# Kernel tuning notes

Measured on AMD Instinct MI355X. Metric: run time of the kernel, lower is better.

## Reference

```python
import jax, jax.numpy as jnp
import numpy as np

N_HEADS = 8
ROPE_BASE = 10000.0


def _rope(x, pos):
    # x: (BN, T, H, D); pos: (T,)
    D = x.shape[-1]
    inv_freq = 1.0 / (ROPE_BASE ** (jnp.arange(0, D, 2, dtype=jnp.float32) / D))  # (D/2,)
    ang = pos[:, None].astype(jnp.float32) * inv_freq[None, :]                    # (T, D/2)
    cos = jnp.concatenate([jnp.cos(ang), jnp.cos(ang)], axis=-1)[None, :, None, :]  # (1,T,1,D)
    sin = jnp.concatenate([jnp.sin(ang), jnp.sin(ang)], axis=-1)[None, :, None, :]
    x1, x2 = x[..., : D // 2], x[..., D // 2 :]
    rot = jnp.concatenate([-x2, x1], axis=-1)
    return x * cos + rot * sin


def setup_inputs() -> dict:
    key = jax.random.key(0)
    ks = jax.random.split(key, 5)
    B, T, N, E = 2, 1024, 4, 256
    s = 1.0 / np.sqrt(E)
    return {
        "input_tensor": jax.random.normal(ks[0], (B, T, N, E), dtype=jnp.float32),
        "w_attn": jax.random.normal(ks[1], (E, 3 * E), dtype=jnp.float32) * s,
        "b_attn": jnp.zeros((3 * E,), dtype=jnp.float32),
        "w_proj": jax.random.normal(ks[2], (E, E), dtype=jnp.float32) * s,
        "b_proj": jnp.zeros((E,), dtype=jnp.float32),
    }


def reference(input_tensor, w_attn, b_attn, w_proj, b_proj):
    B, T, N, E = input_tensor.shape
    H = N_HEADS
    D = E // H
    # (B,T,N,E) -> (B*N, T, E)
    x = jnp.transpose(input_tensor, (0, 2, 1, 3)).reshape(B * N, T, E)
    qkv = x @ w_attn + b_attn  # (BN, T, 3E)
    q, k, v = jnp.split(qkv, 3, axis=-1)
    q = q.reshape(B * N, T, H, D)
    k = k.reshape(B * N, T, H, D)
    v = v.reshape(B * N, T, H, D)
    pos = jnp.arange(T)
    q = _rope(q, pos)
    k = _rope(k, pos)
    # causal SDPA
    scale = 1.0 / jnp.sqrt(jnp.asarray(D, dtype=q.dtype))
    scores = jnp.einsum("bthd,bshd->bhts", q, k) * scale  # (BN,H,T,T)
    causal = jnp.tril(jnp.ones((T, T), dtype=bool))
    scores = jnp.where(causal[None, None], scores, jnp.finfo(scores.dtype).min)
    probs = jax.nn.softmax(scores, axis=-1)
    out = jnp.einsum("bhts,bshd->bthd", probs, v).reshape(B * N, T, E)
    out = out @ w_proj + b_proj
    # (BN,T,E) -> (B,T,N,E)
    return jnp.transpose(out.reshape(B, N, T, E), (0, 2, 1, 3))
```

## Files before the change

kernel.cpp:

```cpp
#include <hip/hip_runtime.h>
#include <hip/hip_bf16.h>

#define T_ 1024
#define NB 4
#define E_ 256
#define H_ 8
#define D_ 32
#define E3 768

typedef __attribute__((ext_vector_type(4))) short v4s;
typedef __attribute__((ext_vector_type(8))) short v8s;
typedef __attribute__((ext_vector_type(4))) float v4f;

#define EXP2F(x) __builtin_amdgcn_exp2f(x)

__device__ __forceinline__ unsigned short f2bf(float x) {
    union { float f; unsigned int u; } v; v.f = x;
    unsigned int r = v.u + 0x7fffu + ((v.u >> 16) & 1u);
    return (unsigned short)(r >> 16);
}
__device__ __forceinline__ unsigned int cvtpk(float lo, float hi) {
    unsigned int r;
    asm("v_cvt_pk_bf16_f32 %0, %1, %2" : "=v"(r) : "v"(lo), "v"(hi));
    return r;
}

__global__ __launch_bounds__(256) void prep_kernel(
    const float* __restrict__ w_attn, const float* __restrict__ w_proj,
    unsigned short* __restrict__ WT, unsigned short* __restrict__ WPT,
    float* __restrict__ ctab, float* __restrict__ stab)
{
    const int blk = blockIdx.x;
    if (blk < 256) {
        __shared__ float tile[32][33];
        const int bx = blk & 31, by = blk >> 5;
        const float* src; unsigned short* dst; int N, n0;
        if (bx < 24) { src = w_attn; dst = WT;  N = 768; n0 = bx * 32; }
        else         { src = w_proj; dst = WPT; N = 256; n0 = (bx - 24) * 32; }
        const int k0 = by * 32;
        const int xx = threadIdx.x & 31, y4 = (threadIdx.x >> 5) * 4;
        #pragma unroll
        for (int i = 0; i < 4; ++i)
            tile[y4 + i][xx] = src[(size_t)(k0 + y4 + i) * N + n0 + xx];
        __syncthreads();
        #pragma unroll
        for (int i = 0; i < 4; ++i)
            dst[(size_t)(n0 + y4 + i) * 256 + k0 + xx] = f2bf(tile[xx][y4 + i]);
    } else {
        const int idx = (blk - 256) * 256 + threadIdx.x;
        const int t = idx >> 4, jj = idx & 15;
        const float invf = __expf(-(float)jj * 0.5756462732485115f);
        float s, c;
        sincosf((float)t * invf, &s, &c);
        ctab[idx] = c;
        stab[idx] = s;
    }
}

__global__ __launch_bounds__(256) void qkv_mfma_kernel(
    const float* __restrict__ x,
    const float* __restrict__ b_attn,
    const unsigned short* __restrict__ WT,
    const float* __restrict__ ctab, const float* __restrict__ stab,
    unsigned short* __restrict__ Qb, unsigned short* __restrict__ Kb,
    unsigned short* __restrict__ VW)
{
    const int tid  = threadIdx.x;
    const int wsb  = tid >> 6;
    const int lane = tid & 63;
    const int g = lane >> 4, c = lane & 15;
    const int m0 = blockIdx.x * 64 + wsb * 16;
    const int n0 = blockIdx.y * 64;
    const int bn = m0 >> 10;
    const int b  = bn >> 2, nidx = bn & 3;
    const int t_base = m0 & 1023;

    const float* xrow = x + ((size_t)(b * T_ + t_base + c) * NB + nidx) * E_;

    v4f acc[4];
    #pragma unroll
    for (int tt = 0; tt < 4; ++tt) acc[tt] = (v4f){0.f, 0.f, 0.f, 0.f};

    #pragma unroll
    for (int k0 = 0; k0 < 256; k0 += 32) {
        float4 f0 = *(const float4*)(xrow + k0 + 8 * g);
        float4 f1 = *(const float4*)(xrow + k0 + 8 * g + 4);
        union { v8s v; uint4 u; } af;
        af.u.x = cvtpk(f0.x, f0.y);
        af.u.y = cvtpk(f0.z, f0.w);
        af.u.z = cvtpk(f1.x, f1.y);
        af.u.w = cvtpk(f1.z, f1.w);
        #pragma unroll
        for (int tt = 0; tt < 4; ++tt) {
            v8s bfrag = *(const v8s*)(WT + (size_t)(n0 + tt * 16 + c) * 256 + k0 + 8 * g);
            acc[tt] = __builtin_amdgcn_mfma_f32_16x16x32_bf16(af.v, bfrag, acc[tt], 0, 0, 0);
        }
    }

    float bias[4];
    #pragma unroll
    for (int tt = 0; tt < 4; ++tt) bias[tt] = b_attn[n0 + tt * 16 + c];

    const int type = n0 >> 8;
    const int nl0  = n0 & 255;

    if (type <= 1) {
        unsigned short* Dst = (type == 0) ? Qb : Kb;
        float sn[4], cs[4];
        #pragma unroll
        for (int r = 0; r < 4; ++r) {
            const int ti = (t_base + 4 * g + r) * 16 + c;
            cs[r] = ctab[ti];
            sn[r] = stab[ti];
        }
        #pragma unroll
        for (int tt = 0; tt < 4; ++tt) {
            const int n_l = nl0 + tt * 16;
            const int h = n_l >> 5, d = (n_l & 31) + c;
            const int bh = bn * 8 + h;
            const float sgn = (tt & 1) ? 1.f : -1.f;
            const int  ptt = tt ^ 1;
            #pragma unroll
            for (int r = 0; r < 4; ++r) {
                float v0 = acc[tt][r] + bias[tt];
                float v1 = acc[ptt][r] + bias[ptt];
                float o  = v0 * cs[r] + sgn * v1 * sn[r];
                int   t  = t_base + 4 * g + r;
                Dst[((size_t)bh * T_ + t) * D_ + d] = f2bf(o);
            }
        }
    } else {
        const int wv_ = t_base >> 5;
        const int tw  = (t_base & 31) + 4 * g;
        const int pos0 = ((tw >> 4) & 1) * 4 + ((tw >> 2) & 3) * 8;
        #pragma unroll
        for (int tt = 0; tt < 4; ++tt) {
            const int n_l = nl0 + tt * 16;
            const int h = n_l >> 5, d = (n_l & 31) + c;
            const int bh = bn * 8 + h;
            ushort4 pk;
            pk.x = f2bf(acc[tt][0] + bias[tt]);
            pk.y = f2bf(acc[tt][1] + bias[tt]);
            pk.z = f2bf(acc[tt][2] + bias[tt]);
            pk.w = f2bf(acc[tt][3] + bias[tt]);
            *(ushort4*)(VW + (((size_t)bh * 32 + wv_) * 32 + d) * 32 + pos0) = pk;
        }
    }
}

#define KMUL   0.2550343f
#define SHIFTL 11.5415603f

__global__ __launch_bounds__(256) void attn_kernel(
    const unsigned short* __restrict__ Qb,
    const unsigned short* __restrict__ Kb,
    const unsigned short* __restrict__ VW,
    unsigned short* __restrict__ Ob)
{
    const int tid  = threadIdx.x;
    const int wv   = tid >> 6;
    const int lane = tid & 63;
    const int g = lane >> 4, c = lane & 15;
    const int bx = blockIdx.x;
    const int bh = bx & 63;
    const int k  = bx >> 6;

    const int qts[2] = { k + 8 * wv, k + 56 - 8 * wv };
    const int lim1 = qts[1] >> 1;

    v8s qf[2];
    #pragma unroll
    for (int j = 0; j < 2; ++j)
        qf[j] = *(const v8s*)(Qb + ((size_t)bh * T_ + qts[j] * 16 + c) * D_ + 8 * g);

    v4f o0[2], o1[2];
    float ll[2];
    #pragma unroll
    for (int j = 0; j < 2; ++j) {
        o0[j] = (v4f){0.f, 0.f, 0.f, 0.f};
        o1[j] = (v4f){0.f, 0.f, 0.f, 0.f};
        ll[j] = 0.f;
    }

    const unsigned short* Ksrc = Kb + (size_t)bh * T_ * D_;
    const unsigned short* Vsrc = VW + (size_t)bh * 32 * 1024;

    const int koff = c * 32 + 8 * g;
    const int voff = c * 32 + 8 * g;

    v8s kA_n  = *(const v8s*)(Ksrc + koff);
    v8s kB_n  = *(const v8s*)(Ksrc + 512 + koff);
    v8s vf0_n = *(const v8s*)(Vsrc + voff);
    v8s vf1_n = *(const v8s*)(Vsrc + 512 + voff);

    for (int w = 0; w <= lim1; ++w) {
        v8s kfA = kA_n, kfB = kB_n;
        v8s vf0 = vf0_n, vf1 = vf1_n;
        if (w < lim1) {
            const unsigned short* kp = Ksrc + (size_t)(w + 1) * 1024;
            const unsigned short* vp = Vsrc + (size_t)(w + 1) * 1024;
            kA_n  = *(const v8s*)(kp + koff);
            kB_n  = *(const v8s*)(kp + 512 + koff);
            vf0_n = *(const v8s*)(vp + voff);
            vf1_n = *(const v8s*)(vp + 512 + voff);
        }

        const int s0 = w * 32;
        #pragma unroll
        for (int j = 0; j < 2; ++j) {
            const int qt  = qts[j];
            const int lim = qt >> 1;
            if (lim < w) continue;
            const int q = qt * 16 + c;

            v4f zero = {0.f, 0.f, 0.f, 0.f};
            v4f sA = __builtin_amdgcn_mfma_f32_16x16x32_bf16(kfA, qf[j], zero, 0, 0, 0);
            v4f sB = __builtin_amdgcn_mfma_f32_16x16x32_bf16(kfB, qf[j], zero, 0, 0, 0);

            const bool diag = (lim == w);
            float p[8];
            #pragma unroll
            for (int r = 0; r < 4; ++r) {
                float pa = EXP2F(fmaf(sA[r], KMUL, -SHIFTL));
                float pb = EXP2F(fmaf(sB[r], KMUL, -SHIFTL));
                if (diag) {
                    if (s0 + 4 * g + r > q)      pa = 0.f;
                    if (s0 + 16 + 4 * g + r > q) pb = 0.f;
                }
                p[r] = pa; p[4 + r] = pb;
                ll[j] += pa + pb;
            }
            union { v8s v; uint4 u; } pu;
            pu.u.x = cvtpk(p[0], p[1]);
            pu.u.y = cvtpk(p[2], p[3]);
            pu.u.z = cvtpk(p[4], p[5]);
            pu.u.w = cvtpk(p[6], p[7]);
            o0[j] = __builtin_amdgcn_mfma_f32_16x16x32_bf16(pu.v, vf0, o0[j], 0, 0, 0);
            o1[j] = __builtin_amdgcn_mfma_f32_16x16x32_bf16(pu.v, vf1, o1[j], 0, 0, 0);
        }
    }

    const int bn = bh >> 3, h = bh & 7;
    #pragma unroll
    for (int j = 0; j < 2; ++j) {
        float l_s = ll[j];
        l_s += __shfl_xor(l_s, 16, 64);
        l_s += __shfl_xor(l_s, 32, 64);
        float linv = 1.0f / l_s;
        float lr[4];
        #pragma unroll
        for (int r = 0; r < 4; ++r) lr[r] = __shfl(linv, 4 * g + r, 64);
        const int q0 = qts[j] * 16;
        #pragma unroll
        for (int r = 0; r < 4; ++r) {
            unsigned short* Orow = Ob + ((size_t)bn * T_ + q0 + 4 * g + r) * E_ + h * D_;
            Orow[c]      = f2bf(o0[j][r] * lr[r]);
            Orow[16 + c] = f2bf(o1[j][r] * lr[r]);
        }
    }
}

__global__ __launch_bounds__(256) void proj_mfma_kernel(
    const unsigned short* __restrict__ Ob,
    const unsigned short* __restrict__ WPT,
    const float* __restrict__ b_proj,
    float* __restrict__ out)
{
    const int tid  = threadIdx.x;
    const int wsb  = tid >> 6;
    const int lane = tid & 63;
    const int g = lane >> 4, c = lane & 15;
    const int m0 = blockIdx.x * 64 + wsb * 16;
    const int n0 = blockIdx.y * 64;
    const int bn = m0 >> 10;
    const int b  = bn >> 2, nidx = bn & 3;
    const int t_base = m0 & 1023;

    const unsigned short* arow = Ob + ((size_t)bn * T_ + t_base + c) * E_;

    v4f acc[4];
    #pragma unroll
    for (int tt = 0; tt < 4; ++tt) acc[tt] = (v4f){0.f, 0.f, 0.f, 0.f};

    #pragma unroll
    for (int s = 0; s < 8; ++s) {
        v8s afrag = *(const v8s*)(arow + s * 32 + 8 * g);
        #pragma unroll
        for (int tt = 0; tt < 4; ++tt) {
            v8s bfrag = *(const v8s*)(WPT + (size_t)(n0 + tt * 16 + c) * 256 + s * 32 + 8 * g);
            acc[tt] = __builtin_amdgcn_mfma_f32_16x16x32_bf16(afrag, bfrag, acc[tt], 0, 0, 0);
        }
    }

    #pragma unroll
    for (int tt = 0; tt < 4; ++tt) {
        const int n = n0 + tt * 16 + c;
        const float bp = b_proj[n];
        #pragma unroll
        for (int r = 0; r < 4; ++r) {
            const int t = t_base + 4 * g + r;
            out[((size_t)(b * T_ + t) * NB + nidx) * E_ + n] = acc[tt][r] + bp;
        }
    }
}

extern "C" void kernel_launch(void* const* d_in, const int* in_sizes, int n_in,
                              void* d_out, int out_size, void* d_ws, size_t ws_size,
                              hipStream_t stream)
{
    const float* x      = (const float*)d_in[0];
    const float* w_attn = (const float*)d_in[1];
    const float* b_attn = (const float*)d_in[2];
    const float* w_proj = (const float*)d_in[3];
    const float* b_proj = (const float*)d_in[4];
    float* out = (float*)d_out;

    unsigned short* Qb  = (unsigned short*)d_ws;
    unsigned short* Kb  = Qb + 2097152;
    unsigned short* VW  = Kb + 2097152;
    unsigned short* Ob  = VW + 2097152;
    unsigned short* WT  = Ob + 2097152;
    unsigned short* WPT = WT + 196608;
    float* ctab = (float*)(WPT + 65536);
    float* stab = ctab + 16384;

    prep_kernel<<<320, 256, 0, stream>>>(w_attn, w_proj, WT, WPT, ctab, stab);
    qkv_mfma_kernel<<<dim3(128, 12), 256, 0, stream>>>(x, b_attn, WT, ctab, stab, Qb, Kb, VW);
    attn_kernel<<<512, 256, 0, stream>>>(Qb, Kb, VW, Ob);
    proj_mfma_kernel<<<dim3(128, 4), 256, 0, stream>>>(Ob, WPT, b_proj, out);
}
```

Baseline: 131.2 us.

## Fuse QKV, attention and projection into one persistent kernel with grid barriers

Merges the QKV GEMM, causal attention and output projection into a single 512-block kernel separated by atomic-counter grid barriers, with the counters reset in the prep kernel. Each block in the QKV phase now computes three 64-column groups, reusing the converted x fragment across them. The goal is to remove two kernel launch gaps and tail effects. In exchange it relies on all 512 blocks being co-resident (launch_bounds 256,2) to avoid deadlock, and it adds spin-wait barrier overhead and more accumulator registers.

```diff
diff --git a/kernel.cpp b/kernel.cpp
--- a/kernel.cpp
+++ b/kernel.cpp
@@ -7,6 +7,7 @@
 #define H_ 8
 #define D_ 32
 #define E3 768
+#define NBLK 512u
 
 typedef __attribute__((ext_vector_type(4))) short v4s;
 typedef __attribute__((ext_vector_type(8))) short v8s;
@@ -25,12 +26,28 @@
     return r;
 }
 
+__device__ __forceinline__ void grid_barrier(unsigned int* cnt) {
+    __syncthreads();
+    __threadfence();
+    if (threadIdx.x == 0) {
+        atomicAdd(cnt, 1u);
+        while (atomicAdd(cnt, 0u) < NBLK) __builtin_amdgcn_s_sleep(2);
+    }
+    __syncthreads();
+    __threadfence();
+}
+
+#define KMUL   0.2550343f
+#define SHIFTL 11.5415603f
+
 __global__ __launch_bounds__(256) void prep_kernel(
     const float* __restrict__ w_attn, const float* __restrict__ w_proj,
     unsigned short* __restrict__ WT, unsigned short* __restrict__ WPT,
-    float* __restrict__ ctab, float* __restrict__ stab)
+    float* __restrict__ ctab, float* __restrict__ stab,
+    unsigned int* __restrict__ cnt)
 {
     const int blk = blockIdx.x;
+    if (blk == 0 && threadIdx.x < 8) cnt[threadIdx.x] = 0u;
     if (blk < 256) {
         __shared__ float tile[32][33];
         const int bx = blk & 31, by = blk >> 5;
@@ -57,55 +74,55 @@
     }
 }
 
-__global__ __launch_bounds__(256) void qkv_mfma_kernel(
+__global__ __launch_bounds__(256, 2) void fused_kernel(
     const float* __restrict__ x,
-    const float* __restrict__ b_attn,
-    const unsigned short* __restrict__ WT,
+    const float* __restrict__ b_attn, const float* __restrict__ b_proj,
+    const unsigned short* __restrict__ WT, const unsigned short* __restrict__ WPT,
     const float* __restrict__ ctab, const float* __restrict__ stab,
     unsigned short* __restrict__ Qb, unsigned short* __restrict__ Kb,
-    unsigned short* __restrict__ VW)
+    unsigned short* __restrict__ VW, unsigned short* __restrict__ Ob,
+    unsigned int* __restrict__ cnt,
+    float* __restrict__ out)
 {
-    const int tid  = threadIdx.x;
+    const int bx  = blockIdx.x;
+    const int tid = threadIdx.x;
     const int wsb  = tid >> 6;
     const int lane = tid & 63;
     const int g = lane >> 4, c = lane & 15;
-    const int m0 = blockIdx.x * 64 + wsb * 16;
-    const int n0 = blockIdx.y * 64;
-    const int bn = m0 >> 10;
-    const int b  = bn >> 2, nidx = bn & 3;
-    const int t_base = m0 & 1023;
-
-    const float* xrow = x + ((size_t)(b * T_ + t_base + c) * NB + nidx) * E_;
-
-    v4f acc[4];
-    #pragma unroll
-    for (int tt = 0; tt < 4; ++tt) acc[tt] = (v4f){0.f, 0.f, 0.f, 0.f};
-
-    #pragma unroll
-    for (int k0 = 0; k0 < 256; k0 += 32) {
-        float4 f0 = *(const float4*)(xrow + k0 + 8 * g);
-        float4 f1 = *(const float4*)(xrow + k0 + 8 * g + 4);
-        union { v8s v; uint4 u; } af;
-        af.u.x = cvtpk(f0.x, f0.y);
-        af.u.y = cvtpk(f0.z, f0.w);
-        af.u.z = cvtpk(f1.x, f1.y);
-        af.u.w = cvtpk(f1.z, f1.w);
-        #pragma unroll
-        for (int tt = 0; tt < 4; ++tt) {
-            v8s bfrag = *(const v8s*)(WT + (size_t)(n0 + tt * 16 + c) * 256 + k0 + 8 * g);
-            acc[tt] = __builtin_amdgcn_mfma_f32_16x16x32_bf16(af.v, bfrag, acc[tt], 0, 0, 0);
-        }
-    }
-
-    float bias[4];
-    #pragma unroll
-    for (int tt = 0; tt < 4; ++tt) bias[tt] = b_attn[n0 + tt * 16 + c];
-
-    const int type = n0 >> 8;
-    const int nl0  = n0 & 255;
-
-    if (type <= 1) {
-        unsigned short* Dst = (type == 0) ? Qb : Kb;
+
+    {
+        const int row = bx & 127, cg0 = (bx >> 7) * 3;
+        const int m0 = row * 64 + wsb * 16;
+        const int bn = m0 >> 10;
+        const int b  = bn >> 2, nidx = bn & 3;
+        const int t_base = m0 & 1023;
+
+        const float* xrow = x + ((size_t)(b * T_ + t_base + c) * NB + nidx) * E_;
+
+        v4f acc[12];
+        #pragma unroll
+        for (int i = 0; i < 12; ++i) acc[i] = (v4f){0.f, 0.f, 0.f, 0.f};
+
+        #pragma unroll
+        for (int k0 = 0; k0 < 256; k0 += 32) {
+            float4 f0 = *(const float4*)(xrow + k0 + 8 * g);
+            float4 f1 = *(const float4*)(xrow + k0 + 8 * g + 4);
+            union { v8s v; uint4 u; } af;
+            af.u.x = cvtpk(f0.x, f0.y);
+            af.u.y = cvtpk(f0.z, f0.w);
+            af.u.z = cvtpk(f1.x, f1.y);
+            af.u.w = cvtpk(f1.z, f1.w);
+            #pragma unroll
+            for (int cc = 0; cc < 3; ++cc) {
+                const int n0 = (cg0 + cc) * 64;
+                #pragma unroll
+                for (int tt = 0; tt < 4; ++tt) {
+                    v8s bfrag = *(const v8s*)(WT + (size_t)(n0 + tt * 16 + c) * 256 + k0 + 8 * g);
+                    acc[cc * 4 + tt] = __builtin_amdgcn_mfma_f32_16x16x32_bf16(af.v, bfrag, acc[cc * 4 + tt], 0, 0, 0);
+                }
+            }
+        }
+
         float sn[4], cs[4];
         #pragma unroll
         for (int r = 0; r < 4; ++r) {
@@ -113,193 +130,191 @@
             cs[r] = ctab[ti];
             sn[r] = stab[ti];
         }
+
+        #pragma unroll
+        for (int cc = 0; cc < 3; ++cc) {
+            const int n0 = (cg0 + cc) * 64;
+            const int type = n0 >> 8;
+            const int nl0  = n0 & 255;
+            float bias[4];
+            #pragma unroll
+            for (int tt = 0; tt < 4; ++tt) bias[tt] = b_attn[n0 + tt * 16 + c];
+
+            if (type <= 1) {
+                unsigned short* Dst = (type == 0) ? Qb : Kb;
+                #pragma unroll
+                for (int tt = 0; tt < 4; ++tt) {
+                    const int n_l = nl0 + tt * 16;
+                    const int h = n_l >> 5, d = (n_l & 31) + c;
+                    const int bh = bn * 8 + h;
+                    const float sgn = (tt & 1) ? 1.f : -1.f;
+                    const int  ptt = tt ^ 1;
+                    #pragma unroll
+                    for (int r = 0; r < 4; ++r) {
+                        float v0 = acc[cc * 4 + tt][r] + bias[tt];
+                        float v1 = acc[cc * 4 + ptt][r] + bias[ptt];
+                        float o  = v0 * cs[r] + sgn * v1 * sn[r];
+                        int   t  = t_base + 4 * g + r;
+                        Dst[((size_t)bh * T_ + t) * D_ + d] = f2bf(o);
+                    }
+                }
+            } else {
+                const int wv_ = t_base >> 5;
+                const int tw  = (t_base & 31) + 4 * g;
+                const int pos0 = ((tw >> 4) & 1) * 4 + ((tw >> 2) & 3) * 8;
+                #pragma unroll
+                for (int tt = 0; tt < 4; ++tt) {
+                    const int n_l = nl0 + tt * 16;
+                    const int h = n_l >> 5, d = (n_l & 31) + c;
+                    const int bh = bn * 8 + h;
+                    ushort4 pk;
+                    pk.x = f2bf(acc[cc * 4 + tt][0] + bias[tt]);
+                    pk.y = f2bf(acc[cc * 4 + tt][1] + bias[tt]);
+                    pk.z = f2bf(acc[cc * 4 + tt][2] + bias[tt]);
+                    pk.w = f2bf(acc[cc * 4 + tt][3] + bias[tt]);
+                    *(ushort4*)(VW + (((size_t)bh * 32 + wv_) * 32 + d) * 32 + pos0) = pk;
+                }
+            }
+        }
+    }
+
+    grid_barrier(cnt + 0);
+
+    {
+        const int wv = wsb;
+        const int bh = bx & 63;
+        const int k  = bx >> 6;
+
+        const int qts[2] = { k + 8 * wv, k + 56 - 8 * wv };
+        const int lim1 = qts[1] >> 1;
+
+        v8s qf[2];
+        #pragma unroll
+        for (int j = 0; j < 2; ++j)
+            qf[j] = *(const v8s*)(Qb + ((size_t)bh * T_ + qts[j] * 16 + c) * D_ + 8 * g);
+
+        v4f o0[2], o1[2];
+        float ll[2];
+        #pragma unroll
+        for (int j = 0; j < 2; ++j) {
+            o0[j] = (v4f){0.f, 0.f, 0.f, 0.f};
+            o1[j] = (v4f){0.f, 0.f, 0.f, 0.f};
+            ll[j] = 0.f;
+        }
+
+        const unsigned short* Ksrc = Kb + (size_t)bh * T_ * D_;
+        const unsigned short* Vsrc = VW + (size_t)bh * 32 * 1024;
+
+        const int koff = c * 32 + 8 * g;
+        const int voff = c * 32 + 8 * g;
+
+        v8s kA_n  = *(const v8s*)(Ksrc + koff);
+        v8s kB_n  = *(const v8s*)(Ksrc + 512 + koff);
+        v8s vf0_n = *(const v8s*)(Vsrc + voff);
+        v8s vf1_n = *(const v8s*)(Vsrc + 512 + voff);
+
+        for (int w = 0; w <= lim1; ++w) {
+            v8s kfA = kA_n, kfB = kB_n;
+            v8s vf0 = vf0_n, vf1 = vf1_n;
+            if (w < lim1) {
+                const unsigned short* kp = Ksrc + (size_t)(w + 1) * 1024;
+                const unsigned short* vp = Vsrc + (size_t)(w + 1) * 1024;
+                kA_n  = *(const v8s*)(kp + koff);
+                kB_n  = *(const v8s*)(kp + 512 + koff);
+                vf0_n = *(const v8s*)(vp + voff);
+                vf1_n = *(const v8s*)(vp + 512 + voff);
+            }
+
+            const int s0 = w * 32;
+            #pragma unroll
+            for (int j = 0; j < 2; ++j) {
+                const int qt  = qts[j];
+                const int lim = qt >> 1;
+                if (lim < w) continue;
+                const int q = qt * 16 + c;
+
+                v4f zero = {0.f, 0.f, 0.f, 0.f};
+                v4f sA = __builtin_amdgcn_mfma_f32_16x16x32_bf16(kfA, qf[j], zero, 0, 0, 0);
+                v4f sB = __builtin_amdgcn_mfma_f32_16x16x32_bf16(kfB, qf[j], zero, 0, 0, 0);
+
+                const bool diag = (lim == w);
+                float p[8];
+                #pragma unroll
+                for (int r = 0; r < 4; ++r) {
+                    float pa = EXP2F(fmaf(sA[r], KMUL, -SHIFTL));
+                    float pb = EXP2F(fmaf(sB[r], KMUL, -SHIFTL));
+                    if (diag) {
+                        if (s0 + 4 * g + r > q)      pa = 0.f;
+                        if (s0 + 16 + 4 * g + r > q) pb = 0.f;
+                    }
+                    p[r] = pa; p[4 + r] = pb;
+                    ll[j] += pa + pb;
+                }
+                union { v8s v; uint4 u; } pu;
+                pu.u.x = cvtpk(p[0], p[1]);
+                pu.u.y = cvtpk(p[2], p[3]);
+                pu.u.z = cvtpk(p[4], p[5]);
+                pu.u.w = cvtpk(p[6], p[7]);
+                o0[j] = __builtin_amdgcn_mfma_f32_16x16x32_bf16(pu.v, vf0, o0[j], 0, 0, 0);
+                o1[j] = __builtin_amdgcn_mfma_f32_16x16x32_bf16(pu.v, vf1, o1[j], 0, 0, 0);
+            }
+        }
+
+        const int bn = bh >> 3, h = bh & 7;
+        #pragma unroll
+        for (int j = 0; j < 2; ++j) {
+            float l_s = ll[j];
+            l_s += __shfl_xor(l_s, 16, 64);
+            l_s += __shfl_xor(l_s, 32, 64);
+            float linv = 1.0f / l_s;
+            float lr[4];
+            #pragma unroll
+            for (int r = 0; r < 4; ++r) lr[r] = __shfl(linv, 4 * g + r, 64);
+            const int q0 = qts[j] * 16;
+            #pragma unroll
+            for (int r = 0; r < 4; ++r) {
+                unsigned short* Orow = Ob + ((size_t)bn * T_ + q0 + 4 * g + r) * E_ + h * D_;
+                Orow[c]      = f2bf(o0[j][r] * lr[r]);
+                Orow[16 + c] = f2bf(o1[j][r] * lr[r]);
+            }
+        }
+    }
+
+    grid_barrier(cnt + 1);
+
+    {
+        const int row = bx & 127, coly = bx >> 7;
+        const int m0 = row * 64 + wsb * 16;
+        const int n0 = coly * 64;
+        const int bn = m0 >> 10;
+        const int b  = bn >> 2, nidx = bn & 3;
+        const int t_base = m0 & 1023;
+
+        const unsigned short* arow = Ob + ((size_t)bn * T_ + t_base + c) * E_;
+
+        v4f acc[4];
+        #pragma unroll
+        for (int tt = 0; tt < 4; ++tt) acc[tt] = (v4f){0.f, 0.f, 0.f, 0.f};
+
+        #pragma unroll
+        for (int s = 0; s < 8; ++s) {
+            v8s afrag = *(const v8s*)(arow + s * 32 + 8 * g);
+            #pragma unroll
+            for (int tt = 0; tt < 4; ++tt) {
+                v8s bfrag = *(const v8s*)(WPT + (size_t)(n0 + tt * 16 + c) * 256 + s * 32 + 8 * g);
+                acc[tt] = __builtin_amdgcn_mfma_f32_16x16x32_bf16(afrag, bfrag, acc[tt], 0, 0, 0);
+            }
+        }
+
         #pragma unroll
         for (int tt = 0; tt < 4; ++tt) {
-            const int n_l = nl0 + tt * 16;
-            const int h = n_l >> 5, d = (n_l & 31) + c;
-            const int bh = bn * 8 + h;
-            const float sgn = (tt & 1) ? 1.f : -1.f;
-            const int  ptt = tt ^ 1;
+            const int n = n0 + tt * 16 + c;
+            const float bp = b_proj[n];
             #pragma unroll
             for (int r = 0; r < 4; ++r) {
-                float v0 = acc[tt][r] + bias[tt];
-                float v1 = acc[ptt][r] + bias[ptt];
-                float o  = v0 * cs[r] + sgn * v1 * sn[r];
-                int   t  = t_base + 4 * g + r;
-                Dst[((size_t)bh * T_ + t) * D_ + d] = f2bf(o);
-            }
-        }
-    } else {
-        const int wv_ = t_base >> 5;
-        const int tw  = (t_base & 31) + 4 * g;
-        const int pos0 = ((tw >> 4) & 1) * 4 + ((tw >> 2) & 3) * 8;
-        #pragma unroll
-        for (int tt = 0; tt < 4; ++tt) {
-            const int n_l = nl0 + tt * 16;
-            const int h = n_l >> 5, d = (n_l & 31) + c;
-            const int bh = bn * 8 + h;
-            ushort4 pk;
-            pk.x = f2bf(acc[tt][0] + bias[tt]);
-            pk.y = f2bf(acc[tt][1] + bias[tt]);
-            pk.z = f2bf(acc[tt][2] + bias[tt]);
-            pk.w = f2bf(acc[tt][3] + bias[tt]);
-            *(ushort4*)(VW + (((size_t)bh * 32 + wv_) * 32 + d) * 32 + pos0) = pk;
-        }
-    }
-}
-
-#define KMUL   0.2550343f
-#define SHIFTL 11.5415603f
-
-__global__ __launch_bounds__(256) void attn_kernel(
-    const unsigned short* __restrict__ Qb,
-    const unsigned short* __restrict__ Kb,
-    const unsigned short* __restrict__ VW,
-    unsigned short* __restrict__ Ob)
-{
-    const int tid  = threadIdx.x;
-    const int wv   = tid >> 6;
-    const int lane = tid & 63;
-    const int g = lane >> 4, c = lane & 15;
-    const int bx = blockIdx.x;
-    const int bh = bx & 63;
-    const int k  = bx >> 6;
-
-    const int qts[2] = { k + 8 * wv, k + 56 - 8 * wv };
-    const int lim1 = qts[1] >> 1;
-
-    v8s qf[2];
-    #pragma unroll
-    for (int j = 0; j < 2; ++j)
-        qf[j] = *(const v8s*)(Qb + ((size_t)bh * T_ + qts[j] * 16 + c) * D_ + 8 * g);
-
-    v4f o0[2], o1[2];
-    float ll[2];
-    #pragma unroll
-    for (int j = 0; j < 2; ++j) {
-        o0[j] = (v4f){0.f, 0.f, 0.f, 0.f};
-        o1[j] = (v4f){0.f, 0.f, 0.f, 0.f};
-        ll[j] = 0.f;
-    }
-
-    const unsigned short* Ksrc = Kb + (size_t)bh * T_ * D_;
-    const unsigned short* Vsrc = VW + (size_t)bh * 32 * 1024;
-
-    const int koff = c * 32 + 8 * g;
-    const int voff = c * 32 + 8 * g;
-
-    v8s kA_n  = *(const v8s*)(Ksrc + koff);
-    v8s kB_n  = *(const v8s*)(Ksrc + 512 + koff);
-    v8s vf0_n = *(const v8s*)(Vsrc + voff);
-    v8s vf1_n = *(const v8s*)(Vsrc + 512 + voff);
-
-    for (int w = 0; w <= lim1; ++w) {
-        v8s kfA = kA_n, kfB = kB_n;
-        v8s vf0 = vf0_n, vf1 = vf1_n;
-        if (w < lim1) {
-            const unsigned short* kp = Ksrc + (size_t)(w + 1) * 1024;
-            const unsigned short* vp = Vsrc + (size_t)(w + 1) * 1024;
-            kA_n  = *(const v8s*)(kp + koff);
-            kB_n  = *(const v8s*)(kp + 512 + koff);
-            vf0_n = *(const v8s*)(vp + voff);
-            vf1_n = *(const v8s*)(vp + 512 + voff);
-        }
-
-        const int s0 = w * 32;
-        #pragma unroll
-        for (int j = 0; j < 2; ++j) {
-            const int qt  = qts[j];
-            const int lim = qt >> 1;
-            if (lim < w) continue;
-            const int q = qt * 16 + c;
-
-            v4f zero = {0.f, 0.f, 0.f, 0.f};
-            v4f sA = __builtin_amdgcn_mfma_f32_16x16x32_bf16(kfA, qf[j], zero, 0, 0, 0);
-            v4f sB = __builtin_amdgcn_mfma_f32_16x16x32_bf16(kfB, qf[j], zero, 0, 0, 0);
-
-            const bool diag = (lim == w);
-            float p[8];
-            #pragma unroll
-            for (int r = 0; r < 4; ++r) {
-                float pa = EXP2F(fmaf(sA[r], KMUL, -SHIFTL));
-                float pb = EXP2F(fmaf(sB[r], KMUL, -SHIFTL));
-                if (diag) {
-                    if (s0 + 4 * g + r > q)      pa = 0.f;
-                    if (s0 + 16 + 4 * g + r > q) pb = 0.f;
-                }
-                p[r] = pa; p[4 + r] = pb;
-                ll[j] += pa + pb;
-            }
-            union { v8s v; uint4 u; } pu;
-            pu.u.x = cvtpk(p[0], p[1]);
-            pu.u.y = cvtpk(p[2], p[3]);
-            pu.u.z = cvtpk(p[4], p[5]);
-            pu.u.w = cvtpk(p[6], p[7]);
-            o0[j] = __builtin_amdgcn_mfma_f32_16x16x32_bf16(pu.v, vf0, o0[j], 0, 0, 0);
-            o1[j] = __builtin_amdgcn_mfma_f32_16x16x32_bf16(pu.v, vf1, o1[j], 0, 0, 0);
-        }
-    }
-
-    const int bn = bh >> 3, h = bh & 7;
-    #pragma unroll
-    for (int j = 0; j < 2; ++j) {
-        float l_s = ll[j];
-        l_s += __shfl_xor(l_s, 16, 64);
-        l_s += __shfl_xor(l_s, 32, 64);
-        float linv = 1.0f / l_s;
-        float lr[4];
-        #pragma unroll
-        for (int r = 0; r < 4; ++r) lr[r] = __shfl(linv, 4 * g + r, 64);
-        const int q0 = qts[j] * 16;
-        #pragma unroll
-        for (int r = 0; r < 4; ++r) {
-            unsigned short* Orow = Ob + ((size_t)bn * T_ + q0 + 4 * g + r) * E_ + h * D_;
-            Orow[c]      = f2bf(o0[j][r] * lr[r]);
-            Orow[16 + c] = f2bf(o1[j][r] * lr[r]);
-        }
-    }
-}
-
-__global__ __launch_bounds__(256) void proj_mfma_kernel(
-    const unsigned short* __restrict__ Ob,
-    const unsigned short* __restrict__ WPT,
-    const float* __restrict__ b_proj,
-    float* __restrict__ out)
-{
-    const int tid  = threadIdx.x;
-    const int wsb  = tid >> 6;
-    const int lane = tid & 63;
-    const int g = lane >> 4, c = lane & 15;
-    const int m0 = blockIdx.x * 64 + wsb * 16;
-    const int n0 = blockIdx.y * 64;
-    const int bn = m0 >> 10;
-    const int b  = bn >> 2, nidx = bn & 3;
-    const int t_base = m0 & 1023;
-
-    const unsigned short* arow = Ob + ((size_t)bn * T_ + t_base + c) * E_;
-
-    v4f acc[4];
-    #pragma unroll
-    for (int tt = 0; tt < 4; ++tt) acc[tt] = (v4f){0.f, 0.f, 0.f, 0.f};
-
-    #pragma unroll
-    for (int s = 0; s < 8; ++s) {
-        v8s afrag = *(const v8s*)(arow + s * 32 + 8 * g);
-        #pragma unroll
-        for (int tt = 0; tt < 4; ++tt) {
-            v8s bfrag = *(const v8s*)(WPT + (size_t)(n0 + tt * 16 + c) * 256 + s * 32 + 8 * g);
-            acc[tt] = __builtin_amdgcn_mfma_f32_16x16x32_bf16(afrag, bfrag, acc[tt], 0, 0, 0);
-        }
-    }
-
-    #pragma unroll
-    for (int tt = 0; tt < 4; ++tt) {
-        const int n = n0 + tt * 16 + c;
-        const float bp = b_proj[n];
-        #pragma unroll
-        for (int r = 0; r < 4; ++r) {
-            const int t = t_base + 4 * g + r;
-            out[((size_t)(b * T_ + t) * NB + nidx) * E_ + n] = acc[tt][r] + bp;
+                const int t = t_base + 4 * g + r;
+                out[((size_t)(b * T_ + t) * NB + nidx) * E_ + n] = acc[tt][r] + bp;
+            }
         }
     }
 }
@@ -323,9 +338,9 @@
     unsigned short* WPT = WT + 196608;
     float* ctab = (float*)(WPT + 65536);
     float* stab = ctab + 16384;
-
-    prep_kernel<<<320, 256, 0, stream>>>(w_attn, w_proj, WT, WPT, ctab, stab);
-    qkv_mfma_kernel<<<dim3(128, 12), 256, 0, stream>>>(x, b_attn, WT, ctab, stab, Qb, Kb, VW);
-    attn_kernel<<<512, 256, 0, stream>>>(Qb, Kb, VW, Ob);
-    proj_mfma_kernel<<<dim3(128, 4), 256, 0, stream>>>(Ob, WPT, b_proj, out);
-}
+    unsigned int* cnt = (unsigned int*)(stab + 16384);
+
+    prep_kernel<<<320, 256, 0, stream>>>(w_attn, w_proj, WT, WPT, ctab, stab, cnt);
+    fused_kernel<<<512, 256, 0, stream>>>(x, b_attn, b_proj, WT, WPT, ctab, stab,
+                                          Qb, Kb, VW, Ob, cnt, out);
+}
```

New measurement: 331.8 us. 153% more time.

## Give each attention wave one query tile and double grid sizes

Applied to the files above, without the earlier changes.

The attention kernel previously gave each wave two paired query tiles (short and long) so the causal work per wave was balanced. Now each wave handles a single 16-row query tile, the grid doubles to 1024 blocks, and heavy tiles are scheduled first. The projection kernel also halves its N tile per block and doubles its grid. The aim is more parallelism and lower register pressure, at the cost of imbalanced per-wave work inside a block and K/V fragments loaded once per tile instead of shared between two tiles.

```diff
diff --git a/kernel.cpp b/kernel.cpp
--- a/kernel.cpp
+++ b/kernel.cpp
@@ -24,6 +24,10 @@
     asm("v_cvt_pk_bf16_f32 %0, %1, %2" : "=v"(r) : "v"(lo), "v"(hi));
     return r;
 }
+
+#define KMUL   0.2550343f
+#define SHIFTL 11.5415603f
+
 
 __global__ __launch_bounds__(256) void prep_kernel(
     const float* __restrict__ w_attn, const float* __restrict__ w_proj,
@@ -148,9 +152,6 @@
     }
 }
 
-#define KMUL   0.2550343f
-#define SHIFTL 11.5415603f
-
 __global__ __launch_bounds__(256) void attn_kernel(
     const unsigned short* __restrict__ Qb,
     const unsigned short* __restrict__ Kb,
@@ -163,24 +164,14 @@
     const int g = lane >> 4, c = lane & 15;
     const int bx = blockIdx.x;
     const int bh = bx & 63;
-    const int k  = bx >> 6;
-
-    const int qts[2] = { k + 8 * wv, k + 56 - 8 * wv };
-    const int lim1 = qts[1] >> 1;
-
-    v8s qf[2];
-    #pragma unroll
-    for (int j = 0; j < 2; ++j)
-        qf[j] = *(const v8s*)(Qb + ((size_t)bh * T_ + qts[j] * 16 + c) * D_ + 8 * g);
-
-    v4f o0[2], o1[2];
-    float ll[2];
-    #pragma unroll
-    for (int j = 0; j < 2; ++j) {
-        o0[j] = (v4f){0.f, 0.f, 0.f, 0.f};
-        o1[j] = (v4f){0.f, 0.f, 0.f, 0.f};
-        ll[j] = 0.f;
-    }
+    const int qt = (15 - (bx >> 6)) + 16 * wv;
+    const int lim = qt >> 1;
+
+    v8s qf = *(const v8s*)(Qb + ((size_t)bh * T_ + qt * 16 + c) * D_ + 8 * g);
+
+    v4f o0 = (v4f){0.f, 0.f, 0.f, 0.f};
+    v4f o1 = (v4f){0.f, 0.f, 0.f, 0.f};
+    float ll = 0.f;
 
     const unsigned short* Ksrc = Kb + (size_t)bh * T_ * D_;
     const unsigned short* Vsrc = VW + (size_t)bh * 32 * 1024;
@@ -193,10 +184,11 @@
     v8s vf0_n = *(const v8s*)(Vsrc + voff);
     v8s vf1_n = *(const v8s*)(Vsrc + 512 + voff);
 
-    for (int w = 0; w <= lim1; ++w) {
+    const int q = qt * 16 + c;
+    for (int w = 0; w <= lim; ++w) {
         v8s kfA = kA_n, kfB = kB_n;
         v8s vf0 = vf0_n, vf1 = vf1_n;
-        if (w < lim1) {
+        if (w < lim) {
             const unsigned short* kp = Ksrc + (size_t)(w + 1) * 1024;
             const unsigned short* vp = Vsrc + (size_t)(w + 1) * 1024;
             kA_n  = *(const v8s*)(kp + koff);
@@ -206,57 +198,46 @@
         }
 
         const int s0 = w * 32;
-        #pragma unroll
-        for (int j = 0; j < 2; ++j) {
-            const int qt  = qts[j];
-            const int lim = qt >> 1;
-            if (lim < w) continue;
-            const int q = qt * 16 + c;
-
-            v4f zero = {0.f, 0.f, 0.f, 0.f};
-            v4f sA = __builtin_amdgcn_mfma_f32_16x16x32_bf16(kfA, qf[j], zero, 0, 0, 0);
-            v4f sB = __builtin_amdgcn_mfma_f32_16x16x32_bf16(kfB, qf[j], zero, 0, 0, 0);
-
-            const bool diag = (lim == w);
-            float p[8];
-            #pragma unroll
-            for (int r = 0; r < 4; ++r) {
-                float pa = EXP2F(fmaf(sA[r], KMUL, -SHIFTL));
-                float pb = EXP2F(fmaf(sB[r], KMUL, -SHIFTL));
-                if (diag) {
-                    if (s0 + 4 * g + r > q)      pa = 0.f;
-                    if (s0 + 16 + 4 * g + r > q) pb = 0.f;
-                }
-                p[r] = pa; p[4 + r] = pb;
-                ll[j] += pa + pb;
+        v4f zero = {0.f, 0.f, 0.f, 0.f};
+        v4f sA = __builtin_amdgcn_mfma_f32_16x16x32_bf16(kfA, qf, zero, 0, 0, 0);
+        v4f sB = __builtin_amdgcn_mfma_f32_16x16x32_bf16(kfB, qf, zero, 0, 0, 0);
+
+        const bool diag = (lim == w);
+        float p[8];
+        #pragma unroll
+        for (int r = 0; r < 4; ++r) {
+            float pa = EXP2F(fmaf(sA[r], KMUL, -SHIFTL));
+            float pb = EXP2F(fmaf(sB[r], KMUL, -SHIFTL));
+            if (diag) {
+                if (s0 + 4 * g + r > q)      pa = 0.f;
+                if (s0 + 16 + 4 * g + r > q) pb = 0.f;
             }
-            union { v8s v; uint4 u; } pu;
-            pu.u.x = cvtpk(p[0], p[1]);
-            pu.u.y = cvtpk(p[2], p[3]);
-            pu.u.z = cvtpk(p[4], p[5]);
-            pu.u.w = cvtpk(p[6], p[7]);
-            o0[j] = __builtin_amdgcn_mfma_f32_16x16x32_bf16(pu.v, vf0, o0[j], 0, 0, 0);
-            o1[j] = __builtin_amdgcn_mfma_f32_16x16x32_bf16(pu.v, vf1, o1[j], 0, 0, 0);
-        }
+            p[r] = pa; p[4 + r] = pb;
+            ll += pa + pb;
+        }
+        union { v8s v; uint4 u; } pu;
+        pu.u.x = cvtpk(p[0], p[1]);
+        pu.u.y = cvtpk(p[2], p[3]);
+        pu.u.z = cvtpk(p[4], p[5]);
+        pu.u.w = cvtpk(p[6], p[7]);
+        o0 = __builtin_amdgcn_mfma_f32_16x16x32_bf16(pu.v, vf0, o0, 0, 0, 0);
+        o1 = __builtin_amdgcn_mfma_f32_16x16x32_bf16(pu.v, vf1, o1, 0, 0, 0);
     }
 
     const int bn = bh >> 3, h = bh & 7;
-    #pragma unroll
-    for (int j = 0; j < 2; ++j) {
-        float l_s = ll[j];
-        l_s += __shfl_xor(l_s, 16, 64);
-        l_s += __shfl_xor(l_s, 32, 64);
-        float linv = 1.0f / l_s;
-        float lr[4];
-        #pragma unroll
-        for (int r = 0; r < 4; ++r) lr[r] = __shfl(linv, 4 * g + r, 64);
-        const int q0 = qts[j] * 16;
-        #pragma unroll
-        for (int r = 0; r < 4; ++r) {
-            unsigned short* Orow = Ob + ((size_t)bn * T_ + q0 + 4 * g + r) * E_ + h * D_;
-            Orow[c]      = f2bf(o0[j][r] * lr[r]);
-            Orow[16 + c] = f2bf(o1[j][r] * lr[r]);
-        }
+    float l_s = ll;
+    l_s += __shfl_xor(l_s, 16, 64);
+    l_s += __shfl_xor(l_s, 32, 64);
+    float linv = 1.0f / l_s;
+    float lr[4];
+    #pragma unroll
+    for (int r = 0; r < 4; ++r) lr[r] = __shfl(linv, 4 * g + r, 64);
+    const int q0 = qt * 16;
+    #pragma unroll
+    for (int r = 0; r < 4; ++r) {
+        unsigned short* Orow = Ob + ((size_t)bn * T_ + q0 + 4 * g + r) * E_ + h * D_;
+        Orow[c]      = f2bf(o0[r] * lr[r]);
+        Orow[16 + c] = f2bf(o1[r] * lr[r]);
     }
 }
 
@@ -271,29 +252,29 @@
     const int lane = tid & 63;
     const int g = lane >> 4, c = lane & 15;
     const int m0 = blockIdx.x * 64 + wsb * 16;
-    const int n0 = blockIdx.y * 64;
+    const int n0 = blockIdx.y * 32;
     const int bn = m0 >> 10;
     const int b  = bn >> 2, nidx = bn & 3;
     const int t_base = m0 & 1023;
 
     const unsigned short* arow = Ob + ((size_t)bn * T_ + t_base + c) * E_;
 
-    v4f acc[4];
-    #pragma unroll
-    for (int tt = 0; tt < 4; ++tt) acc[tt] = (v4f){0.f, 0.f, 0.f, 0.f};
+    v4f acc[2];
+    #pragma unroll
+    for (int tt = 0; tt < 2; ++tt) acc[tt] = (v4f){0.f, 0.f, 0.f, 0.f};
 
     #pragma unroll
     for (int s = 0; s < 8; ++s) {
         v8s afrag = *(const v8s*)(arow + s * 32 + 8 * g);
         #pragma unroll
-        for (int tt = 0; tt < 4; ++tt) {
+        for (int tt = 0; tt < 2; ++tt) {
             v8s bfrag = *(const v8s*)(WPT + (size_t)(n0 + tt * 16 + c) * 256 + s * 32 + 8 * g);
             acc[tt] = __builtin_amdgcn_mfma_f32_16x16x32_bf16(afrag, bfrag, acc[tt], 0, 0, 0);
         }
     }
 
     #pragma unroll
-    for (int tt = 0; tt < 4; ++tt) {
+    for (int tt = 0; tt < 2; ++tt) {
         const int n = n0 + tt * 16 + c;
         const float bp = b_proj[n];
         #pragma unroll
@@ -326,6 +307,6 @@
 
     prep_kernel<<<320, 256, 0, stream>>>(w_attn, w_proj, WT, WPT, ctab, stab);
     qkv_mfma_kernel<<<dim3(128, 12), 256, 0, stream>>>(x, b_attn, WT, ctab, stab, Qb, Kb, VW);
-    attn_kernel<<<512, 256, 0, stream>>>(Qb, Kb, VW, Ob);
-    proj_mfma_kernel<<<dim3(128, 4), 256, 0, stream>>>(Ob, WPT, b_proj, out);
-}
+    attn_kernel<<<1024, 256, 0, stream>>>(Qb, Kb, VW, Ob);
+    proj_mfma_kernel<<<dim3(128, 8), 256, 0, stream>>>(Ob, WPT, b_proj, out);
+}
```

After: 134.5 us. +2.5%, slower.

## Fuse weight transpose and RoPE table into GEMM kernels, drop prep kernel

Applied to the files above, without the earlier changes.

Removes the separate prep kernel. Each QKV and projection block now loads its 64-column slice of the fp32 weights, converts it to bf16 and transposes it into padded shared memory, then reads B fragments from LDS. The RoPE sin/cos values are computed inline instead of read from precomputed tables. This saves one launch and a global round trip, at the cost of every block redoing the weight conversion (128x redundant weight reads) and a shared-memory staging sync.

```diff
diff --git a/kernel.cpp b/kernel.cpp
--- a/kernel.cpp
+++ b/kernel.cpp
@@ -8,7 +8,6 @@
 #define D_ 32
 #define E3 768
 
-typedef __attribute__((ext_vector_type(4))) short v4s;
 typedef __attribute__((ext_vector_type(8))) short v8s;
 typedef __attribute__((ext_vector_type(4))) float v4f;
 
@@ -25,46 +24,19 @@
     return r;
 }
 
-__global__ __launch_bounds__(256) void prep_kernel(
-    const float* __restrict__ w_attn, const float* __restrict__ w_proj,
-    unsigned short* __restrict__ WT, unsigned short* __restrict__ WPT,
-    float* __restrict__ ctab, float* __restrict__ stab)
-{
-    const int blk = blockIdx.x;
-    if (blk < 256) {
-        __shared__ float tile[32][33];
-        const int bx = blk & 31, by = blk >> 5;
-        const float* src; unsigned short* dst; int N, n0;
-        if (bx < 24) { src = w_attn; dst = WT;  N = 768; n0 = bx * 32; }
-        else         { src = w_proj; dst = WPT; N = 256; n0 = (bx - 24) * 32; }
-        const int k0 = by * 32;
-        const int xx = threadIdx.x & 31, y4 = (threadIdx.x >> 5) * 4;
-        #pragma unroll
-        for (int i = 0; i < 4; ++i)
-            tile[y4 + i][xx] = src[(size_t)(k0 + y4 + i) * N + n0 + xx];
-        __syncthreads();
-        #pragma unroll
-        for (int i = 0; i < 4; ++i)
-            dst[(size_t)(n0 + y4 + i) * 256 + k0 + xx] = f2bf(tile[xx][y4 + i]);
-    } else {
-        const int idx = (blk - 256) * 256 + threadIdx.x;
-        const int t = idx >> 4, jj = idx & 15;
-        const float invf = __expf(-(float)jj * 0.5756462732485115f);
-        float s, c;
-        sincosf((float)t * invf, &s, &c);
-        ctab[idx] = c;
-        stab[idx] = s;
-    }
-}
+#define KMUL   0.2550343f
+#define SHIFTL 11.5415603f
+
 
 __global__ __launch_bounds__(256) void qkv_mfma_kernel(
     const float* __restrict__ x,
+    const float* __restrict__ w_attn,
     const float* __restrict__ b_attn,
-    const unsigned short* __restrict__ WT,
-    const float* __restrict__ ctab, const float* __restrict__ stab,
     unsigned short* __restrict__ Qb, unsigned short* __restrict__ Kb,
     unsigned short* __restrict__ VW)
 {
+    __shared__ unsigned short WTs[64][264];
+
     const int tid  = threadIdx.x;
     const int wsb  = tid >> 6;
     const int lane = tid & 63;
@@ -75,6 +47,21 @@
     const int b  = bn >> 2, nidx = bn & 3;
     const int t_base = m0 & 1023;
 
+    {
+        const int c4 = (tid & 15) * 4;
+        const int kr = tid >> 4;
+        #pragma unroll
+        for (int p = 0; p < 16; ++p) {
+            const int k = p * 16 + kr;
+            float4 w4 = *(const float4*)(w_attn + (size_t)k * E3 + n0 + c4);
+            WTs[c4 + 0][k] = f2bf(w4.x);
+            WTs[c4 + 1][k] = f2bf(w4.y);
+            WTs[c4 + 2][k] = f2bf(w4.z);
+            WTs[c4 + 3][k] = f2bf(w4.w);
+        }
+    }
+    __syncthreads();
+
     const float* xrow = x + ((size_t)(b * T_ + t_base + c) * NB + nidx) * E_;
 
     v4f acc[4];
@@ -92,7 +79,7 @@
         af.u.w = cvtpk(f1.z, f1.w);
         #pragma unroll
         for (int tt = 0; tt < 4; ++tt) {
-            v8s bfrag = *(const v8s*)(WT + (size_t)(n0 + tt * 16 + c) * 256 + k0 + 8 * g);
+            v8s bfrag = *(const v8s*)(&WTs[tt * 16 + c][k0 + 8 * g]);
             acc[tt] = __builtin_amdgcn_mfma_f32_16x16x32_bf16(af.v, bfrag, acc[tt], 0, 0, 0);
         }
     }
@@ -107,11 +94,11 @@
     if (type <= 1) {
         unsigned short* Dst = (type == 0) ? Qb : Kb;
         float sn[4], cs[4];
-        #pragma unroll
-        for (int r = 0; r < 4; ++r) {
-            const int ti = (t_base + 4 * g + r) * 16 + c;
-            cs[r] = ctab[ti];
-            sn[r] = stab[ti];
+        {
+            const float invf = __expf(-(float)c * 0.5756462732485115f);
+            #pragma unroll
+            for (int r = 0; r < 4; ++r)
+                sincosf((float)(t_base + 4 * g + r) * invf, &sn[r], &cs[r]);
         }
         #pragma unroll
         for (int tt = 0; tt < 4; ++tt) {
@@ -147,9 +134,6 @@
         }
     }
 }
-
-#define KMUL   0.2550343f
-#define SHIFTL 11.5415603f
 
 __global__ __launch_bounds__(256) void attn_kernel(
     const unsigned short* __restrict__ Qb,
@@ -262,10 +246,12 @@
 
 __global__ __launch_bounds__(256) void proj_mfma_kernel(
     const unsigned short* __restrict__ Ob,
-    const unsigned short* __restrict__ WPT,
+    const float* __restrict__ w_proj,
     const float* __restrict__ b_proj,
     float* __restrict__ out)
 {
+    __shared__ unsigned short WPs[64][264];
+
     const int tid  = threadIdx.x;
     const int wsb  = tid >> 6;
     const int lane = tid & 63;
@@ -276,6 +262,21 @@
     const int b  = bn >> 2, nidx = bn & 3;
     const int t_base = m0 & 1023;
 
+    {
+        const int c4 = (tid & 15) * 4;
+        const int kr = tid >> 4;
+        #pragma unroll
+        for (int p = 0; p < 16; ++p) {
+            const int k = p * 16 + kr;
+            float4 w4 = *(const float4*)(w_proj + (size_t)k * E_ + n0 + c4);
+            WPs[c4 + 0][k] = f2bf(w4.x);
+            WPs[c4 + 1][k] = f2bf(w4.y);
+            WPs[c4 + 2][k] = f2bf(w4.z);
+            WPs[c4 + 3][k] = f2bf(w4.w);
+        }
+    }
+    __syncthreads();
+
     const unsigned short* arow = Ob + ((size_t)bn * T_ + t_base + c) * E_;
 
     v4f acc[4];
@@ -287,7 +288,7 @@
         v8s afrag = *(const v8s*)(arow + s * 32 + 8 * g);
         #pragma unroll
         for (int tt = 0; tt < 4; ++tt) {
-            v8s bfrag = *(const v8s*)(WPT + (size_t)(n0 + tt * 16 + c) * 256 + s * 32 + 8 * g);
+            v8s bfrag = *(const v8s*)(&WPs[tt * 16 + c][s * 32 + 8 * g]);
             acc[tt] = __builtin_amdgcn_mfma_f32_16x16x32_bf16(afrag, bfrag, acc[tt], 0, 0, 0);
         }
     }
@@ -319,13 +320,8 @@
     unsigned short* Kb  = Qb + 2097152;
     unsigned short* VW  = Kb + 2097152;
     unsigned short* Ob  = VW + 2097152;
-    unsigned short* WT  = Ob + 2097152;
-    unsigned short* WPT = WT + 196608;
-    float* ctab = (float*)(WPT + 65536);
-    float* stab = ctab + 16384;
-
-    prep_kernel<<<320, 256, 0, stream>>>(w_attn, w_proj, WT, WPT, ctab, stab);
-    qkv_mfma_kernel<<<dim3(128, 12), 256, 0, stream>>>(x, b_attn, WT, ctab, stab, Qb, Kb, VW);
+
+    qkv_mfma_kernel<<<dim3(128, 12), 256, 0, stream>>>(x, w_attn, b_attn, Qb, Kb, VW);
     attn_kernel<<<512, 256, 0, stream>>>(Qb, Kb, VW, Ob);
-    proj_mfma_kernel<<<dim3(128, 4), 256, 0, stream>>>(Ob, WPT, b_proj, out);
-}
+    proj_mfma_kernel<<<dim3(128, 4), 256, 0, stream>>>(Ob, w_proj, b_proj, out);
+}
```

Measured after the change: 110.1 us (median of 2 runs). -16.1%, faster.
